# Kernel optimization log

Measured on AMD Instinct MI355X. Metric: run time of the kernel, lower is better.

## Reference

```python
import jax, jax.numpy as jnp
import numpy as np
from jax import lax

B, L, T, H = 8192, 1024, 32, 32  # batch, input length, time steps, lstm hidden
EPS = 1e-5


def _conv1d(x, w, stride, pad):
    # x: [N, C, L], w: [O, I, K]
    return lax.conv_general_dilated(x, w, (stride,), [(pad, pad)],
                                    dimension_numbers=('NCH', 'OIH', 'NCH'))


def _bn(x, g, be, m, v):
    # eval-mode batchnorm over channel dim of [N, C, L]
    inv = g / jnp.sqrt(v + EPS)
    return x * inv[None, :, None] + (be - m * inv)[None, :, None]


def setup_inputs() -> dict:
    key = jax.random.key(0)
    ks = jax.random.split(key, 32)
    r = lambda i, shape, s=0.1: jax.random.normal(ks[i], shape, jnp.float32) * s
    u = lambda i, shape: jax.random.uniform(ks[i], shape, jnp.float32, 0.5, 1.5)
    return {
        'x': jax.random.normal(ks[0], (B, L, 1), jnp.float32),
        'w1': r(1, (8, 1, 7)), 'b1': r(2, (8,)), 'g1': u(3, (8,)), 'be1': r(4, (8,)),
        'm1': r(5, (8,)), 'v1': u(6, (8,)),
        'w2': r(7, (16, 8, 5)), 'b2': r(8, (16,)), 'g2': u(9, (16,)), 'be2': r(10, (16,)),
        'm2': r(11, (16,)), 'v2': u(12, (16,)),
        'w3': r(13, (32, 16, 3)), 'b3': r(14, (32,)), 'g3': u(15, (32,)), 'be3': r(16, (32,)),
        'm3': r(17, (32,)), 'v3': u(18, (32,)),
        'w_ih': r(19, (4 * H, 32)), 'w_hh': r(20, (4 * H, H)),
        'b_ih': r(21, (4 * H,)), 'b_hh': r(22, (4 * H,)),
        'fc1w': r(23, (64, 64)), 'fc1b': r(24, (64,)),
        'fc2w': r(25, (32, 64)), 'fc2b': r(26, (32,)),
        'fc3w': r(27, (4, 32)), 'fc3b': r(28, (4,)),
    }


def _forward(x, w1, b1, g1, be1, m1, v1, w2, b2, g2, be2, m2, v2,
             w3, b3, g3, be3, m3, v3, w_ih, w_hh, b_ih, b_hh,
             fc1w, fc1b, fc2w, fc2b, fc3w, fc3b):
    bsz = x.shape[0]
    h = x.transpose(0, 2, 1)                      # [B, 1, 1024]
    h = jax.nn.relu(_bn(_conv1d(h, w1, 4, 3) + b1[None, :, None], g1, be1, m1, v1))
    h = jax.nn.relu(_bn(_conv1d(h, w2, 4, 2) + b2[None, :, None], g2, be2, m2, v2))
    h = jax.nn.relu(_bn(_conv1d(h, w3, 2, 1) + b3[None, :, None], g3, be3, m3, v3))
    # h: [B, 32, 32]
    spatial = h.mean(axis=2)                      # [B, 32]
    snn_in = h.transpose(0, 2, 1).reshape(bsz, T, -1)  # [B, 32, 32]

    # LIF neuron: sequential decay/threshold/reset scan over time
    def lif_step(mem, xt):
        mem = 0.9 * mem + xt
        spike = (mem > 0.5).astype(xt.dtype)
        mem = mem * (1.0 - spike)
        return mem, spike

    _, spikes = lax.scan(lif_step, jnp.zeros((bsz, snn_in.shape[2]), snn_in.dtype),
                         snn_in.transpose(1, 0, 2))  # spikes: [T, B, F]

    # single-layer LSTM, keep only last hidden state
    def lstm_step(carry, xt):
        hh, cc = carry
        gates = xt @ w_ih.T + b_ih + hh @ w_hh.T + b_hh
        i, f, g, o = jnp.split(gates, 4, axis=1)
        cc = jax.nn.sigmoid(f) * cc + jax.nn.sigmoid(i) * jnp.tanh(g)
        hh = jax.nn.sigmoid(o) * jnp.tanh(cc)
        return (hh, cc), None

    init = (jnp.zeros((bsz, H), x.dtype), jnp.zeros((bsz, H), x.dtype))
    (h_last, _), _ = lax.scan(lstm_step, init, spikes)

    combined = jnp.concatenate([h_last, spatial], axis=1)  # [B, 64]
    z = jax.nn.relu(combined @ fc1w.T + fc1b)
    z = jax.nn.relu(z @ fc2w.T + fc2b)
    out = z @ fc3w.T + fc3b                                # [B, 4]
    return out, spatial, h_last


def reference(x, w1, b1, g1, be1, m1, v1, w2, b2, g2, be2, m2, v2,
              w3, b3, g3, be3, m3, v3, w_ih, w_hh, b_ih, b_hh,
              fc1w, fc1b, fc2w, fc2b, fc3w, fc3b):
    return _forward(x, w1, b1, g1, be1, m1, v1, w2, b2, g2, be2, m2, v2,
                    w3, b3, g3, be3, m3, v3, w_ih, w_hh, b_ih, b_hh,
                    fc1w, fc1b, fc2w, fc2b, fc3w, fc3b)
```

## Files before the change

kernel.cpp:

```cpp
#include <hip/hip_runtime.h>

#define NB 8192
#define EPS_BN 1e-5f

#define PADX(i) ((i) + ((((i) >> 5)) << 2))

using bf16x8 = __attribute__((ext_vector_type(8))) __bf16;
using bf16x4 = __attribute__((ext_vector_type(4))) __bf16;
using f32x4  = __attribute__((ext_vector_type(4))) float;
using f32x2  = __attribute__((ext_vector_type(2))) float;
using u32x4  = __attribute__((ext_vector_type(4))) unsigned int;

#define WSF_OFF 262144
#define PK_WIH  2560
#define PK_WHH  4608
#define PK_FC1  6656
#define PK_FC2  8704
#define PK_FC3  9728
#define PK_BFR  9984
#define PK_B1   10112
#define PK_B2   10176
#define PK_B3   10208
#define PK_SPB  12288

__device__ inline unsigned pack_bf16(float a, float b) {
    union { __bf16 h; unsigned short u; } ca, cb;
    ca.h = (__bf16)a; cb.h = (__bf16)b;
    return (unsigned)ca.u | ((unsigned)cb.u << 16);
}

__global__ __launch_bounds__(256) void fold_kernel(
    const float* __restrict__ w1, const float* __restrict__ b1,
    const float* __restrict__ g1, const float* __restrict__ be1,
    const float* __restrict__ m1, const float* __restrict__ v1,
    const float* __restrict__ w2, const float* __restrict__ b2,
    const float* __restrict__ g2, const float* __restrict__ be2,
    const float* __restrict__ m2, const float* __restrict__ v2,
    const float* __restrict__ w3, const float* __restrict__ b3,
    const float* __restrict__ g3, const float* __restrict__ be3,
    const float* __restrict__ m3, const float* __restrict__ v3,
    const float* __restrict__ w_ih, const float* __restrict__ w_hh,
    const float* __restrict__ b_ih, const float* __restrict__ b_hh,
    const float* __restrict__ fc1w, const float* __restrict__ fc1b,
    const float* __restrict__ fc2w, const float* __restrict__ fc2b,
    const float* __restrict__ fc3w, const float* __restrict__ fc3b,
    float* __restrict__ wsf)
{
    int j = blockIdx.x * 256 + threadIdx.x;
    if (j < 64) {
        int k = j >> 3, c = j & 7;
        wsf[j] = (k < 7) ? w1[c * 7 + k] * (g1[c] * rsqrtf(v1[c] + EPS_BN)) : 0.f;
    } else if (j < 72) {
        int c = j - 64;
        float inv = g1[c] * rsqrtf(v1[c] + EPS_BN);
        wsf[j] = (b1[c] - m1[c]) * inv + be1[c];
    } else if (j >= 80 && j < 720) {
        int i = j - 80, c = i & 15, t = i >> 4, ci = t / 5, k = t - 5 * ci;
        wsf[j] = w2[(c * 8 + ci) * 5 + k] * (g2[c] * rsqrtf(v2[c] + EPS_BN));
    } else if (j >= 720 && j < 736) {
        int c = j - 720;
        float inv = g2[c] * rsqrtf(v2[c] + EPS_BN);
        wsf[j] = (b2[c] - m2[c]) * inv + be2[c];
    } else if (j >= 736 && j < 2272) {
        int i = j - 736, c = i & 31, t = i >> 5, ci = t / 3, k = t - 3 * ci;
        wsf[j] = w3[(c * 16 + ci) * 3 + k] * (g3[c] * rsqrtf(v3[c] + EPS_BN));
    } else if (j >= 2272 && j < 2304) {
        int c = j - 2272;
        float inv = g3[c] * rsqrtf(v3[c] + EPS_BN);
        wsf[j] = (b3[c] - m3[c]) * inv + be3[c];
    } else if (j >= 2560 && j < 3072) {
        int idx = j - 2560, T = idx >> 6, j6 = idx & 63, row = j6 & 15, q = j6 >> 4;
        const float* src = w_ih + (size_t)(16 * T + row) * 32 + 8 * q;
        unsigned* dst = (unsigned*)(wsf + PK_WIH) + (size_t)idx * 4;
        #pragma unroll
        for (int i = 0; i < 4; i++) dst[i] = pack_bf16(src[2 * i], src[2 * i + 1]);
    } else if (j >= 3072 && j < 3584) {
        int idx = j - 3072, T = idx >> 6, j6 = idx & 63, row = j6 & 15, q = j6 >> 4;
        const float* src = w_hh + (size_t)(16 * T + row) * 32 + 8 * q;
        unsigned* dst = (unsigned*)(wsf + PK_WHH) + (size_t)idx * 4;
        #pragma unroll
        for (int i = 0; i < 4; i++) dst[i] = pack_bf16(src[2 * i], src[2 * i + 1]);
    } else if (j >= 3584 && j < 4096) {
        int idx = j - 3584, f = idx >> 6, j6 = idx & 63, row = j6 & 15, q = j6 >> 4;
        int T = f >> 1, s = f & 1;
        const float* src = fc1w + (size_t)(16 * T + row) * 64 + 32 * s + 8 * q;
        unsigned* dst = (unsigned*)(wsf + PK_FC1) + (size_t)idx * 4;
        #pragma unroll
        for (int i = 0; i < 4; i++) dst[i] = pack_bf16(src[2 * i], src[2 * i + 1]);
    } else if (j >= 4096 && j < 4352) {
        int idx = j - 4096, f = idx >> 6, j6 = idx & 63, row = j6 & 15, q = j6 >> 4;
        int T = f >> 1, s = f & 1;
        const float* src = fc2w + (size_t)(16 * T + row) * 64 + 32 * s + 8 * q;
        unsigned* dst = (unsigned*)(wsf + PK_FC2) + (size_t)idx * 4;
        #pragma unroll
        for (int i = 0; i < 4; i++) dst[i] = pack_bf16(src[2 * i], src[2 * i + 1]);
    } else if (j >= 4352 && j < 4416) {
        int j6 = j - 4352, row = j6 & 15, q = j6 >> 4;
        const float* src = fc3w + (size_t)(row & 3) * 32 + 8 * q;
        unsigned* dst = (unsigned*)(wsf + PK_FC3) + (size_t)j6 * 4;
        #pragma unroll
        for (int i = 0; i < 4; i++) dst[i] = pack_bf16(src[2 * i], src[2 * i + 1]);
    } else if (j >= 4416 && j < 4448) {
        int idx = j - 4416, T = idx >> 2, q = idx & 3;
        #pragma unroll
        for (int i = 0; i < 4; i++)
            wsf[PK_BFR + idx * 4 + i] = b_ih[16 * T + 4 * q + i] + b_hh[16 * T + 4 * q + i];
    } else if (j >= 4448 && j < 4464) {
        int idx = j - 4448, T = idx >> 2, q = idx & 3;
        #pragma unroll
        for (int i = 0; i < 4; i++) wsf[PK_B1 + idx * 4 + i] = fc1b[16 * T + 4 * q + i];
    } else if (j >= 4464 && j < 4472) {
        int idx = j - 4464, T = idx >> 2, q = idx & 3;
        #pragma unroll
        for (int i = 0; i < 4; i++) wsf[PK_B2 + idx * 4 + i] = fc2b[16 * T + 4 * q + i];
    } else if (j == 4472) {
        #pragma unroll
        for (int i = 0; i < 4; i++) wsf[PK_B3 + i] = fc3b[i];
    }
}

__device__ inline f32x2 pkfma(f32x2 a, f32x2 b, f32x2 c) {
    return __builtin_elementwise_fma(a, b, c);
}

__device__ inline void conv1_pos(float* __restrict__ c1t,
                                 const float* __restrict__ xb,
                                 const float* __restrict__ wsf,
                                 int p, int idx)
{
    float4 gb = *reinterpret_cast<const float4*>(xb + 4 * p);
    float4 ga = make_float4(0.f, 0.f, 0.f, 0.f);
    if (p > 0) ga = *reinterpret_cast<const float4*>(xb + 4 * p - 4);
    float win[7] = {ga.y, ga.z, ga.w, gb.x, gb.y, gb.z, gb.w};
    #pragma unroll
    for (int cp = 0; cp < 4; cp++) {
        f32x2 acc = *reinterpret_cast<const f32x2*>(wsf + 64 + 2 * cp);
        #pragma unroll
        for (int k = 0; k < 7; k++) {
            f32x2 wv = *reinterpret_cast<const f32x2*>(wsf + k * 8 + 2 * cp);
            f32x2 sv = {win[k], win[k]};
            acc = pkfma(wv, sv, acc);
        }
        c1t[(2 * cp + 0) * 148 + PADX(idx)] = fmaxf(acc[0], 0.f);
        c1t[(2 * cp + 1) * 148 + PADX(idx)] = fmaxf(acc[1], 0.f);
    }
}

__global__ __launch_bounds__(256) void conv_lif_kernel(
    const float* __restrict__ x,
    float* __restrict__ wsf,
    float* __restrict__ spatial_out,
    unsigned int* __restrict__ spk)
{
    __shared__ alignas(16) float smem[4812];
    float* const c1b = smem;
    float* const c3b = smem;
    float* const c2b = smem + 2376;

    const int b0  = blockIdx.x * 2;
    const int tid = threadIdx.x;
    const float* xg0 = x + (size_t)b0 * 1024;
    const float* xg1 = x + (size_t)(b0 + 1) * 1024;

    #pragma unroll
    for (int h = 0; h < 2; h++) {
        {
            const int be = tid >> 7;
            const int lp = tid & 127;
            const float* xb = be ? xg1 : xg0;
            float* c1t = c1b + be * 1188;
            const int p = 126 * h + lp;
            conv1_pos(c1t, xb, wsf, p, p + 2 - 128 * h);
            if (h == 1 && lp == 0)
                conv1_pos(c1t, xb, wsf, 254, 128);
            if (h == 0 && lp < 2) {
                #pragma unroll
                for (int ch = 0; ch < 8; ch++) c1t[ch * 148 + lp] = 0.f;
            }
        }
        __syncthreads();

        {
            const int Pl = tid & 31;
            const int be = (tid >> 5) & 1;
            const int cq = __builtin_amdgcn_readfirstlane(tid >> 6) << 2;
            const int P  = 32 * h + Pl;
            const float* wB2 = wsf + 80;
            const float* bB2 = wsf + 720;
            f32x2 a01 = *reinterpret_cast<const f32x2*>(bB2 + cq);
            f32x2 a23 = *reinterpret_cast<const f32x2*>(bB2 + cq + 2);
            const float* c1t = c1b + be * 1188;
            float* c2t = c2b + be * 1220;
            if (h == 0 && Pl == 0) {
                #pragma unroll
                for (int j = 0; j < 4; j++) c2t[(cq + j) * 76] = 0.f;
            }
            #pragma unroll
            for (int ci = 0; ci < 8; ci++) {
                const float* row = c1t + ci * 148;
                float4 va = *reinterpret_cast<const float4*>(&row[PADX(4 * Pl)]);
                float  v4 = row[PADX(4 * Pl + 4)];
                float win[5] = {va.x, va.y, va.z, va.w, v4};
                #pragma unroll
                for (int k = 0; k < 5; k++) {
                    const float* wp = wB2 + (ci * 5 + k) * 16 + cq;
                    f32x2 sv = {win[k], win[k]};
                    a01 = pkfma(*reinterpret_cast<const f32x2*>(wp),     sv, a01);
                    a23 = pkfma(*reinterpret_cast<const f32x2*>(wp + 2), sv, a23);
                }
            }
            c2t[(cq + 0) * 76 + PADX(1 + P)] = fmaxf(a01[0], 0.f);
            c2t[(cq + 1) * 76 + PADX(1 + P)] = fmaxf(a01[1], 0.f);
            c2t[(cq + 2) * 76 + PADX(1 + P)] = fmaxf(a23[0], 0.f);
            c2t[(cq + 3) * 76 + PADX(1 + P)] = fmaxf(a23[1], 0.f);
        }
        __syncthreads();
    }

    {
        const int pl  = tid & 63;
        const int be  = pl >> 5;
        const int pos = pl & 31;
        const int cb  = __builtin_amdgcn_readfirstlane(tid >> 6) << 3;
        const float* wC3 = wsf + 736;
        const float* bC3 = wsf + 2272;
        f32x2 a01 = *reinterpret_cast<const f32x2*>(bC3 + cb);
        f32x2 a23 = *reinterpret_cast<const f32x2*>(bC3 + cb + 2);
        f32x2 a45 = *reinterpret_cast<const f32x2*>(bC3 + cb + 4);
        f32x2 a67 = *reinterpret_cast<const f32x2*>(bC3 + cb + 6);
        const float* c2t = c2b + be * 1220;
        #pragma unroll
        for (int ci = 0; ci < 16; ci++) {
            const float* row = c2t + ci * 76;
            float2 vab = *reinterpret_cast<const float2*>(&row[PADX(2 * pos)]);
            float  vc  = row[PADX(2 * pos + 2)];
            float win[3] = {vab.x, vab.y, vc};
            #pragma unroll
            for (int k = 0; k < 3; k++) {
                const float* wp = wC3 + (ci * 3 + k) * 32 + cb;
                f32x2 sv = {win[k], win[k]};
                a01 = pkfma(*reinterpret_cast<const f32x2*>(wp),     sv, a01);
                a23 = pkfma(*reinterpret_cast<const f32x2*>(wp + 2), sv, a23);
                a45 = pkfma(*reinterpret_cast<const f32x2*>(wp + 4), sv, a45);
                a67 = pkfma(*reinterpret_cast<const f32x2*>(wp + 6), sv, a67);
            }
        }
        float* c3t = c3b + be * 1060;
        c3t[(cb + 0) * 33 + pos] = fmaxf(a01[0], 0.f);
        c3t[(cb + 1) * 33 + pos] = fmaxf(a01[1], 0.f);
        c3t[(cb + 2) * 33 + pos] = fmaxf(a23[0], 0.f);
        c3t[(cb + 3) * 33 + pos] = fmaxf(a23[1], 0.f);
        c3t[(cb + 4) * 33 + pos] = fmaxf(a45[0], 0.f);
        c3t[(cb + 5) * 33 + pos] = fmaxf(a45[1], 0.f);
        c3t[(cb + 6) * 33 + pos] = fmaxf(a67[0], 0.f);
        c3t[(cb + 7) * 33 + pos] = fmaxf(a67[1], 0.f);
    }
    __syncthreads();

    if (tid < 64) {
        const int be = tid >> 5, ch = tid & 31;
        const float* c3t = c3b + be * 1060;
        float s = 0.f;
        #pragma unroll
        for (int t = 0; t < 32; t++) s += c3t[ch * 33 + t];
        float sv = s * 0.03125f;
        spatial_out[(size_t)(b0 + be) * 32 + ch] = sv;
        union { __bf16 h; unsigned short u; } cv;
        cv.h = (__bf16)sv;
        ((unsigned short*)(wsf + PK_SPB))[(size_t)(b0 + be) * 32 + ch] = cv.u;

        float mem = 0.f;
        #pragma unroll
        for (int t = 0; t < 32; t++) {
            mem = __fadd_rn(__fmul_rn(0.9f, mem), c3t[ch * 33 + t]);
            bool spike = mem > 0.5f;
            mem = spike ? 0.f : mem;
            unsigned long long msk = __ballot(spike);
            if (tid == 0) {
                spk[(size_t)b0 * 32 + t]      = (unsigned int)(msk & 0xffffffffull);
                spk[(size_t)b0 * 32 + 32 + t] = (unsigned int)(msk >> 32);
            }
        }
    }
}

__device__ inline float sigm(float x) {
    return __builtin_amdgcn_rcpf(1.f + __expf(-x));
}
__device__ inline float tanh_(float x) {
    return fmaf(2.f, __builtin_amdgcn_rcpf(1.f + __expf(-2.f * x)), -1.f);
}

__global__ __launch_bounds__(256, 2) void lstm_fc_mfma_kernel(
    const unsigned int* __restrict__ spk,
    const float* __restrict__ wsf,
    float* __restrict__ out0,
    float* __restrict__ hlast_out)
{
    const int ltid = threadIdx.x;
    const int l    = ltid & 63;
    const int g    = ltid >> 6;
    const int row  = l & 15;
    const int q    = l >> 4;
    const int base = blockIdx.x * 16;

    __shared__ unsigned int mlds[512];
    __shared__ alignas(16) __bf16 hdb[640];
    __shared__ alignas(16) float  actb[2304];
    __shared__ alignas(16) __bf16 zlds[1152];

    for (int i = ltid; i < 512; i += 256) {
        int j = i >> 5, t = i & 31;
        mlds[t * 16 + j] = spk[(size_t)(base + j) * 32 + t];
    }
    for (int i = ltid; i < 640; i += 256) hdb[i] = (__bf16)0.f;

    union bc { u32x4 u; bf16x8 v; };
    const u32x4* wihp = (const u32x4*)(wsf + PK_WIH);
    const u32x4* whhp = (const u32x4*)(wsf + PK_WHH);

    const int T0 = 2 * g, T1 = 2 * g + 1;
    bf16x8 wih0, wih1, whh0, whh1;
    { bc a; a.u = wihp[T0 * 64 + l]; wih0 = a.v; }
    { bc a; a.u = wihp[T1 * 64 + l]; wih1 = a.v; }
    { bc a; a.u = whhp[T0 * 64 + l]; whh0 = a.v; }
    { bc a; a.u = whhp[T1 * 64 + l]; whh1 = a.v; }
    f32x4 bfr0 = *reinterpret_cast<const f32x4*>(wsf + PK_BFR + (T0 * 4 + q) * 4);
    f32x4 bfr1 = *reinterpret_cast<const f32x4*>(wsf + PK_BFR + (T1 * 4 + q) * 4);

    const float as = (g == 2) ? 2.f : 1.f;
    const float am = (g == 2) ? 2.f : 1.f;
    const float ac = (g == 2) ? -1.f : 0.f;

    const int crow = ltid & 15, cci = ltid >> 4;
    float cst0 = 0.f, cst1 = 0.f, h0 = 0.f, h1 = 0.f;

    __syncthreads();

    #pragma unroll 1
    for (int t = 0; t < 32; t++) {
        unsigned int m  = mlds[t * 16 + row];
        unsigned int by = (m >> (q * 8)) & 0xFFu;
        union { bf16x8 v; unsigned int u[4]; } a1;
        a1.u[0] = ((by & 1u)        * 0x3F80u) | (((by >> 1) & 1u) * 0x3F800000u);
        a1.u[1] = (((by >> 2) & 1u) * 0x3F80u) | (((by >> 3) & 1u) * 0x3F800000u);
        a1.u[2] = (((by >> 4) & 1u) * 0x3F80u) | (((by >> 5) & 1u) * 0x3F800000u);
        a1.u[3] = (((by >> 6) & 1u) * 0x3F80u) | (((by >> 7) & 1u) * 0x3F800000u);
        bf16x8 a2 = *reinterpret_cast<bf16x8*>(&hdb[row * 40 + q * 8]);

        f32x4 acc0 = __builtin_amdgcn_mfma_f32_16x16x32_bf16(wih0, a1.v, bfr0, 0, 0, 0);
        acc0       = __builtin_amdgcn_mfma_f32_16x16x32_bf16(whh0, a2,   acc0, 0, 0, 0);
        f32x4 acc1 = __builtin_amdgcn_mfma_f32_16x16x32_bf16(wih1, a1.v, bfr1, 0, 0, 0);
        acc1       = __builtin_amdgcn_mfma_f32_16x16x32_bf16(whh1, a2,   acc1, 0, 0, 0);

        f32x4 e0, e1;
        #pragma unroll
        for (int j = 0; j < 4; j++) {
            e0[j] = fmaf(am, sigm(as * acc0[j]), ac);
            e1[j] = fmaf(am, sigm(as * acc1[j]), ac);
        }
        *reinterpret_cast<f32x4*>(&actb[g * 576 + row * 36 + 4 * q])      = e0;
        *reinterpret_cast<f32x4*>(&actb[g * 576 + row * 36 + 16 + 4 * q]) = e1;
        __syncthreads();

        {
            float iv0 = actb[0 * 576 + crow * 36 + cci];
            float fv0 = actb[1 * 576 + crow * 36 + cci];
            float gv0 = actb[2 * 576 + crow * 36 + cci];
            float ov0 = actb[3 * 576 + crow * 36 + cci];
            float iv1 = actb[0 * 576 + crow * 36 + 16 + cci];
            float fv1 = actb[1 * 576 + crow * 36 + 16 + cci];
            float gv1 = actb[2 * 576 + crow * 36 + 16 + cci];
            float ov1 = actb[3 * 576 + crow * 36 + 16 + cci];
            cst0 = fmaf(fv0, cst0, iv0 * gv0);
            h0   = ov0 * tanh_(cst0);
            cst1 = fmaf(fv1, cst1, iv1 * gv1);
            h1   = ov1 * tanh_(cst1);
            hdb[crow * 40 + cci]      = (__bf16)h0;
            hdb[crow * 40 + 16 + cci] = (__bf16)h1;
        }
        __syncthreads();
    }

    hlast_out[(size_t)(base + crow) * 32 + cci]      = h0;
    hlast_out[(size_t)(base + crow) * 32 + 16 + cci] = h1;

    bf16x8 hf = *reinterpret_cast<bf16x8*>(&hdb[row * 40 + 8 * q]);
    bf16x8 spf;
    {
        bc s_;
        s_.u = *reinterpret_cast<const u32x4*>(
            (const unsigned short*)(wsf + PK_SPB) + (size_t)(base + row) * 32 + 8 * q);
        spf = s_.v;
    }

    const u32x4* fc1p = (const u32x4*)(wsf + PK_FC1);
    {
        const int T = g;
        bc x0_, x1_;
        x0_.u = fc1p[(T * 2 + 0) * 64 + l];
        x1_.u = fc1p[(T * 2 + 1) * 64 + l];
        f32x4 c = *reinterpret_cast<const f32x4*>(wsf + PK_B1 + (T * 4 + q) * 4);
        f32x4 a = __builtin_amdgcn_mfma_f32_16x16x32_bf16(x0_.v, hf,  c, 0, 0, 0);
        a       = __builtin_amdgcn_mfma_f32_16x16x32_bf16(x1_.v, spf, a, 0, 0, 0);
        bf16x4 zv;
        #pragma unroll
        for (int i = 0; i < 4; i++) zv[i] = (__bf16)fmaxf(a[i], 0.f);
        *reinterpret_cast<bf16x4*>(&zlds[row * 72 + 16 * T + 4 * q]) = zv;
    }
    __syncthreads();
    bf16x8 z1f0 = *reinterpret_cast<bf16x8*>(&zlds[row * 72 + 8 * q]);
    bf16x8 z1f1 = *reinterpret_cast<bf16x8*>(&zlds[row * 72 + 32 + 8 * q]);

    __bf16* z2b = (__bf16*)actb;
    const u32x4* fc2p = (const u32x4*)(wsf + PK_FC2);
    if (g < 2) {
        const int T = g;
        bc x0_, x1_;
        x0_.u = fc2p[(T * 2 + 0) * 64 + l];
        x1_.u = fc2p[(T * 2 + 1) * 64 + l];
        f32x4 c = *reinterpret_cast<const f32x4*>(wsf + PK_B2 + (T * 4 + q) * 4);
        f32x4 a = __builtin_amdgcn_mfma_f32_16x16x32_bf16(x0_.v, z1f0, c, 0, 0, 0);
        a       = __builtin_amdgcn_mfma_f32_16x16x32_bf16(x1_.v, z1f1, a, 0, 0, 0);
        bf16x4 zv;
        #pragma unroll
        for (int i = 0; i < 4; i++) zv[i] = (__bf16)fmaxf(a[i], 0.f);
        *reinterpret_cast<bf16x4*>(&z2b[row * 40 + 16 * T + 4 * q]) = zv;
    }
    __syncthreads();

    if (g == 0) {
        bf16x8 z2f = *reinterpret_cast<bf16x8*>(&z2b[row * 40 + 8 * q]);
        bc x3_;
        x3_.u = ((const u32x4*)(wsf + PK_FC3))[l];
        f32x4 c = *reinterpret_cast<const f32x4*>(wsf + PK_B3);
        f32x4 o = __builtin_amdgcn_mfma_f32_16x16x32_bf16(x3_.v, z2f, c, 0, 0, 0);
        if (l < 16)
            *reinterpret_cast<f32x4*>(out0 + (size_t)(base + row) * 4) = o;
    }
}

extern "C" void kernel_launch(void* const* d_in, const int* in_sizes, int n_in,
                              void* d_out, int out_size, void* d_ws, size_t ws_size,
                              hipStream_t stream) {
    const float* x    = (const float*)d_in[0];
    const float* w1   = (const float*)d_in[1];
    const float* b1   = (const float*)d_in[2];
    const float* g1   = (const float*)d_in[3];
    const float* be1  = (const float*)d_in[4];
    const float* m1   = (const float*)d_in[5];
    const float* v1   = (const float*)d_in[6];
    const float* w2   = (const float*)d_in[7];
    const float* b2   = (const float*)d_in[8];
    const float* g2   = (const float*)d_in[9];
    const float* be2  = (const float*)d_in[10];
    const float* m2   = (const float*)d_in[11];
    const float* v2   = (const float*)d_in[12];
    const float* w3   = (const float*)d_in[13];
    const float* b3   = (const float*)d_in[14];
    const float* g3   = (const float*)d_in[15];
    const float* be3  = (const float*)d_in[16];
    const float* m3   = (const float*)d_in[17];
    const float* v3   = (const float*)d_in[18];
    const float* w_ih = (const float*)d_in[19];
    const float* w_hh = (const float*)d_in[20];
    const float* b_ih = (const float*)d_in[21];
    const float* b_hh = (const float*)d_in[22];
    const float* fc1w = (const float*)d_in[23];
    const float* fc1b = (const float*)d_in[24];
    const float* fc2w = (const float*)d_in[25];
    const float* fc2b = (const float*)d_in[26];
    const float* fc3w = (const float*)d_in[27];
    const float* fc3b = (const float*)d_in[28];

    float* out0    = (float*)d_out;
    float* spatial = out0 + (size_t)NB * 4;
    float* hlast   = spatial + (size_t)NB * 32;
    unsigned int* spk = (unsigned int*)d_ws;
    float* wsf = (float*)d_ws + WSF_OFF;

    hipLaunchKernelGGL(fold_kernel, dim3(18), dim3(256), 0, stream,
                       w1, b1, g1, be1, m1, v1,
                       w2, b2, g2, be2, m2, v2,
                       w3, b3, g3, be3, m3, v3,
                       w_ih, w_hh, b_ih, b_hh,
                       fc1w, fc1b, fc2w, fc2b, fc3w, fc3b, wsf);

    hipLaunchKernelGGL(conv_lif_kernel, dim3(NB / 2), dim3(256), 0, stream,
                       x, wsf, spatial, spk);

    hipLaunchKernelGGL(lstm_fc_mfma_kernel, dim3(NB / 16), dim3(256), 0, stream,
                       spk, wsf, out0, hlast);
}
```

Baseline: 63.14 us.

## Restructure conv kernel to one wavefront per sample with per-thread multi-output work

Switches the conv+LIF kernel from 256-thread blocks covering two samples to 64-thread single-wavefront blocks covering one sample. Each thread now computes 4 conv1 positions and all output channels for conv2 and conv3, holding more accumulators in registers. The intent is to cut block-wide barrier cost, shrink shared memory per block and raise the compute done per load. In exchange each thread carries more register pressure and the launch has twice as many blocks. The conv3 stage still runs on all 64 lanes, but only the first 32 lanes write their results.

```diff
diff --git a/kernel.cpp b/kernel.cpp
--- a/kernel.cpp
+++ b/kernel.cpp
@@ -123,163 +123,137 @@
     return __builtin_elementwise_fma(a, b, c);
 }
 
-__device__ inline void conv1_pos(float* __restrict__ c1t,
-                                 const float* __restrict__ xb,
-                                 const float* __restrict__ wsf,
-                                 int p, int idx)
-{
-    float4 gb = *reinterpret_cast<const float4*>(xb + 4 * p);
-    float4 ga = make_float4(0.f, 0.f, 0.f, 0.f);
-    if (p > 0) ga = *reinterpret_cast<const float4*>(xb + 4 * p - 4);
-    float win[7] = {ga.y, ga.z, ga.w, gb.x, gb.y, gb.z, gb.w};
-    #pragma unroll
-    for (int cp = 0; cp < 4; cp++) {
-        f32x2 acc = *reinterpret_cast<const f32x2*>(wsf + 64 + 2 * cp);
-        #pragma unroll
-        for (int k = 0; k < 7; k++) {
-            f32x2 wv = *reinterpret_cast<const f32x2*>(wsf + k * 8 + 2 * cp);
-            f32x2 sv = {win[k], win[k]};
-            acc = pkfma(wv, sv, acc);
-        }
-        c1t[(2 * cp + 0) * 148 + PADX(idx)] = fmaxf(acc[0], 0.f);
-        c1t[(2 * cp + 1) * 148 + PADX(idx)] = fmaxf(acc[1], 0.f);
-    }
-}
-
-__global__ __launch_bounds__(256) void conv_lif_kernel(
+__global__ __launch_bounds__(64) void conv_lif_kernel(
     const float* __restrict__ x,
-    float* __restrict__ wsf,
+    const float* __restrict__ wsf,
+    unsigned short* __restrict__ spb,
     float* __restrict__ spatial_out,
     unsigned int* __restrict__ spk)
 {
-    __shared__ alignas(16) float smem[4812];
-    float* const c1b = smem;
-    float* const c3b = smem;
-    float* const c2b = smem + 2376;
-
-    const int b0  = blockIdx.x * 2;
-    const int tid = threadIdx.x;
-    const float* xg0 = x + (size_t)b0 * 1024;
-    const float* xg1 = x + (size_t)(b0 + 1) * 1024;
-
-    #pragma unroll
-    for (int h = 0; h < 2; h++) {
-        {
-            const int be = tid >> 7;
-            const int lp = tid & 127;
-            const float* xb = be ? xg1 : xg0;
-            float* c1t = c1b + be * 1188;
-            const int p = 126 * h + lp;
-            conv1_pos(c1t, xb, wsf, p, p + 2 - 128 * h);
-            if (h == 1 && lp == 0)
-                conv1_pos(c1t, xb, wsf, 254, 128);
-            if (h == 0 && lp < 2) {
+    __shared__ alignas(16) float smem[3552];
+    float* const c1 = smem;
+    float* const c3 = smem;
+    float* const c2 = smem + 2336;
+
+    const int b = blockIdx.x;
+    const int l = threadIdx.x;
+    const float* xb = x + (size_t)b * 1024;
+
+    if (l < 8) { c1[l * 292] = 0.f; c1[l * 292 + 1] = 0.f; }
+    if (l < 16) c2[l * 76] = 0.f;
+
+    {
+        float4 xv0 = make_float4(0.f, 0.f, 0.f, 0.f);
+        if (l > 0) xv0 = *reinterpret_cast<const float4*>(xb + 16 * l - 4);
+        float4 xv1 = *reinterpret_cast<const float4*>(xb + 16 * l);
+        float4 xv2 = *reinterpret_cast<const float4*>(xb + 16 * l + 4);
+        float4 xv3 = *reinterpret_cast<const float4*>(xb + 16 * l + 8);
+        float4 xv4 = *reinterpret_cast<const float4*>(xb + 16 * l + 12);
+        float xw[20] = {xv0.x, xv0.y, xv0.z, xv0.w,
+                        xv1.x, xv1.y, xv1.z, xv1.w,
+                        xv2.x, xv2.y, xv2.z, xv2.w,
+                        xv3.x, xv3.y, xv3.z, xv3.w,
+                        xv4.x, xv4.y, xv4.z, xv4.w};
+        #pragma unroll
+        for (int i = 0; i < 4; i++) {
+            const int p = 4 * l + i;
+            #pragma unroll
+            for (int cp = 0; cp < 4; cp++) {
+                f32x2 acc = *reinterpret_cast<const f32x2*>(wsf + 64 + 2 * cp);
                 #pragma unroll
-                for (int ch = 0; ch < 8; ch++) c1t[ch * 148 + lp] = 0.f;
+                for (int k = 0; k < 7; k++) {
+                    f32x2 wv = *reinterpret_cast<const f32x2*>(wsf + k * 8 + 2 * cp);
+                    f32x2 sv = {xw[4 * i + 1 + k], xw[4 * i + 1 + k]};
+                    acc = pkfma(wv, sv, acc);
+                }
+                c1[(2 * cp + 0) * 292 + PADX(2 + p)] = fmaxf(acc[0], 0.f);
+                c1[(2 * cp + 1) * 292 + PADX(2 + p)] = fmaxf(acc[1], 0.f);
             }
         }
-        __syncthreads();
-
-        {
-            const int Pl = tid & 31;
-            const int be = (tid >> 5) & 1;
-            const int cq = __builtin_amdgcn_readfirstlane(tid >> 6) << 2;
-            const int P  = 32 * h + Pl;
-            const float* wB2 = wsf + 80;
-            const float* bB2 = wsf + 720;
-            f32x2 a01 = *reinterpret_cast<const f32x2*>(bB2 + cq);
-            f32x2 a23 = *reinterpret_cast<const f32x2*>(bB2 + cq + 2);
-            const float* c1t = c1b + be * 1188;
-            float* c2t = c2b + be * 1220;
-            if (h == 0 && Pl == 0) {
+    }
+    __syncthreads();
+
+    {
+        const float* wB2 = wsf + 80;
+        const float* bB2 = wsf + 720;
+        f32x2 a[8];
+        #pragma unroll
+        for (int pr = 0; pr < 8; pr++)
+            a[pr] = *reinterpret_cast<const f32x2*>(bB2 + 2 * pr);
+        #pragma unroll
+        for (int ci = 0; ci < 8; ci++) {
+            const float* row = c1 + ci * 292;
+            float4 va = *reinterpret_cast<const float4*>(&row[PADX(4 * l)]);
+            float  v4 = row[PADX(4 * l + 4)];
+            float win[5] = {va.x, va.y, va.z, va.w, v4};
+            #pragma unroll
+            for (int k = 0; k < 5; k++) {
+                const float* wp = wB2 + (ci * 5 + k) * 16;
+                f32x2 sv = {win[k], win[k]};
                 #pragma unroll
-                for (int j = 0; j < 4; j++) c2t[(cq + j) * 76] = 0.f;
+                for (int pr = 0; pr < 8; pr++)
+                    a[pr] = pkfma(*reinterpret_cast<const f32x2*>(wp + 2 * pr), sv, a[pr]);
             }
-            #pragma unroll
-            for (int ci = 0; ci < 8; ci++) {
-                const float* row = c1t + ci * 148;
-                float4 va = *reinterpret_cast<const float4*>(&row[PADX(4 * Pl)]);
-                float  v4 = row[PADX(4 * Pl + 4)];
-                float win[5] = {va.x, va.y, va.z, va.w, v4};
-                #pragma unroll
-                for (int k = 0; k < 5; k++) {
-                    const float* wp = wB2 + (ci * 5 + k) * 16 + cq;
-                    f32x2 sv = {win[k], win[k]};
-                    a01 = pkfma(*reinterpret_cast<const f32x2*>(wp),     sv, a01);
-                    a23 = pkfma(*reinterpret_cast<const f32x2*>(wp + 2), sv, a23);
-                }
-            }
-            c2t[(cq + 0) * 76 + PADX(1 + P)] = fmaxf(a01[0], 0.f);
-            c2t[(cq + 1) * 76 + PADX(1 + P)] = fmaxf(a01[1], 0.f);
-            c2t[(cq + 2) * 76 + PADX(1 + P)] = fmaxf(a23[0], 0.f);
-            c2t[(cq + 3) * 76 + PADX(1 + P)] = fmaxf(a23[1], 0.f);
-        }
-        __syncthreads();
-    }
+        }
+        #pragma unroll
+        for (int pr = 0; pr < 8; pr++) {
+            c2[(2 * pr + 0) * 76 + PADX(1 + l)] = fmaxf(a[pr][0], 0.f);
+            c2[(2 * pr + 1) * 76 + PADX(1 + l)] = fmaxf(a[pr][1], 0.f);
+        }
+    }
+    __syncthreads();
 
     {
-        const int pl  = tid & 63;
-        const int be  = pl >> 5;
-        const int pos = pl & 31;
-        const int cb  = __builtin_amdgcn_readfirstlane(tid >> 6) << 3;
+        const int p3 = l & 31;
         const float* wC3 = wsf + 736;
         const float* bC3 = wsf + 2272;
-        f32x2 a01 = *reinterpret_cast<const f32x2*>(bC3 + cb);
-        f32x2 a23 = *reinterpret_cast<const f32x2*>(bC3 + cb + 2);
-        f32x2 a45 = *reinterpret_cast<const f32x2*>(bC3 + cb + 4);
-        f32x2 a67 = *reinterpret_cast<const f32x2*>(bC3 + cb + 6);
-        const float* c2t = c2b + be * 1220;
+        f32x2 a[16];
+        #pragma unroll
+        for (int pr = 0; pr < 16; pr++)
+            a[pr] = *reinterpret_cast<const f32x2*>(bC3 + 2 * pr);
         #pragma unroll
         for (int ci = 0; ci < 16; ci++) {
-            const float* row = c2t + ci * 76;
-            float2 vab = *reinterpret_cast<const float2*>(&row[PADX(2 * pos)]);
-            float  vc  = row[PADX(2 * pos + 2)];
+            const float* row = c2 + ci * 76;
+            float2 vab = *reinterpret_cast<const float2*>(&row[PADX(2 * p3)]);
+            float  vc  = row[PADX(2 * p3 + 2)];
             float win[3] = {vab.x, vab.y, vc};
             #pragma unroll
             for (int k = 0; k < 3; k++) {
-                const float* wp = wC3 + (ci * 3 + k) * 32 + cb;
+                const float* wp = wC3 + (ci * 3 + k) * 32;
                 f32x2 sv = {win[k], win[k]};
-                a01 = pkfma(*reinterpret_cast<const f32x2*>(wp),     sv, a01);
-                a23 = pkfma(*reinterpret_cast<const f32x2*>(wp + 2), sv, a23);
-                a45 = pkfma(*reinterpret_cast<const f32x2*>(wp + 4), sv, a45);
-                a67 = pkfma(*reinterpret_cast<const f32x2*>(wp + 6), sv, a67);
+                #pragma unroll
+                for (int pr = 0; pr < 16; pr++)
+                    a[pr] = pkfma(*reinterpret_cast<const f32x2*>(wp + 2 * pr), sv, a[pr]);
             }
         }
-        float* c3t = c3b + be * 1060;
-        c3t[(cb + 0) * 33 + pos] = fmaxf(a01[0], 0.f);
-        c3t[(cb + 1) * 33 + pos] = fmaxf(a01[1], 0.f);
-        c3t[(cb + 2) * 33 + pos] = fmaxf(a23[0], 0.f);
-        c3t[(cb + 3) * 33 + pos] = fmaxf(a23[1], 0.f);
-        c3t[(cb + 4) * 33 + pos] = fmaxf(a45[0], 0.f);
-        c3t[(cb + 5) * 33 + pos] = fmaxf(a45[1], 0.f);
-        c3t[(cb + 6) * 33 + pos] = fmaxf(a67[0], 0.f);
-        c3t[(cb + 7) * 33 + pos] = fmaxf(a67[1], 0.f);
-    }
-    __syncthreads();
-
-    if (tid < 64) {
-        const int be = tid >> 5, ch = tid & 31;
-        const float* c3t = c3b + be * 1060;
+        if (l < 32) {
+            #pragma unroll
+            for (int pr = 0; pr < 16; pr++) {
+                c3[(2 * pr + 0) * 33 + p3] = fmaxf(a[pr][0], 0.f);
+                c3[(2 * pr + 1) * 33 + p3] = fmaxf(a[pr][1], 0.f);
+            }
+        }
+    }
+    __syncthreads();
+
+    if (l < 32) {
         float s = 0.f;
         #pragma unroll
-        for (int t = 0; t < 32; t++) s += c3t[ch * 33 + t];
+        for (int t = 0; t < 32; t++) s += c3[l * 33 + t];
         float sv = s * 0.03125f;
-        spatial_out[(size_t)(b0 + be) * 32 + ch] = sv;
+        spatial_out[(size_t)b * 32 + l] = sv;
         union { __bf16 h; unsigned short u; } cv;
         cv.h = (__bf16)sv;
-        ((unsigned short*)(wsf + PK_SPB))[(size_t)(b0 + be) * 32 + ch] = cv.u;
+        spb[(size_t)b * 32 + l] = cv.u;
 
         float mem = 0.f;
         #pragma unroll
         for (int t = 0; t < 32; t++) {
-            mem = __fadd_rn(__fmul_rn(0.9f, mem), c3t[ch * 33 + t]);
+            mem = __fadd_rn(__fmul_rn(0.9f, mem), c3[l * 33 + t]);
             bool spike = mem > 0.5f;
             mem = spike ? 0.f : mem;
             unsigned long long msk = __ballot(spike);
-            if (tid == 0) {
-                spk[(size_t)b0 * 32 + t]      = (unsigned int)(msk & 0xffffffffull);
-                spk[(size_t)b0 * 32 + 32 + t] = (unsigned int)(msk >> 32);
-            }
+            if (l == 0) spk[(size_t)b * 32 + t] = (unsigned int)(msk & 0xffffffffull);
         }
     }
 }
@@ -478,6 +452,7 @@
     float* hlast   = spatial + (size_t)NB * 32;
     unsigned int* spk = (unsigned int*)d_ws;
     float* wsf = (float*)d_ws + WSF_OFF;
+    unsigned short* spb = (unsigned short*)(wsf + PK_SPB);
 
     hipLaunchKernelGGL(fold_kernel, dim3(18), dim3(256), 0, stream,
                        w1, b1, g1, be1, m1, v1,
@@ -486,8 +461,8 @@
                        w_ih, w_hh, b_ih, b_hh,
                        fc1w, fc1b, fc2w, fc2b, fc3w, fc3b, wsf);
 
-    hipLaunchKernelGGL(conv_lif_kernel, dim3(NB / 2), dim3(256), 0, stream,
-                       x, wsf, spatial, spk);
+    hipLaunchKernelGGL(conv_lif_kernel, dim3(NB), dim3(64), 0, stream,
+                       x, wsf, spb, spatial, spk);
 
     hipLaunchKernelGGL(lstm_fc_mfma_kernel, dim3(NB / 16), dim3(256), 0, stream,
                        spk, wsf, out0, hlast);
```

After: 79.94 us. +26.6%, slower.
